# Optimization experiments

Hardware: AMD Instinct MI355X
Metric: run time of the kernel (lower is better)

## Reference

```python
import jax, jax.numpy as jnp
import numpy as np

N_QUBITS = 6
N_QLAYERS = 3
CNOT = jnp.array([[1,0,0,0],[0,1,0,0],[0,0,0,1],[0,0,1,0]], dtype=jnp.complex64).reshape(2,2,2,2)


def _rx(t):
    c = jnp.cos(0.5 * t).astype(jnp.complex64)
    s = jnp.sin(0.5 * t).astype(jnp.complex64)
    return jnp.stack([jnp.stack([c, -1j * s]), jnp.stack([-1j * s, c])])


def _ry(t):
    c = jnp.cos(0.5 * t).astype(jnp.complex64)
    s = jnp.sin(0.5 * t).astype(jnp.complex64)
    return jnp.stack([jnp.stack([c, -s]), jnp.stack([s, c])])


def _rz(t):
    e0 = jnp.exp(-0.5j * t)
    e1 = jnp.exp(0.5j * t)
    z = jnp.zeros((), jnp.complex64)
    return jnp.stack([jnp.stack([e0, z]), jnp.stack([z, e1])])


def _apply1(state, U, wire):
    st = jnp.tensordot(U, state, axes=([1], [wire]))
    return jnp.moveaxis(st, 0, wire)


def _apply_cnot(state, c, t):
    st = jnp.tensordot(CNOT, state, axes=([2, 3], [c, t]))
    return jnp.moveaxis(st, (0, 1), (c, t))


def _circuit(inputs, weights):
    # 6-qubit statevector sim of the PennyLane circuit; inputs: [6], weights: [3,6]
    state = jnp.zeros((2,) * N_QUBITS, jnp.complex64).at[(0,) * N_QUBITS].set(1.0)
    for i in range(N_QUBITS):
        state = _apply1(state, _rx(inputs[i % N_QUBITS]), i)
        state = _apply1(state, _ry(inputs[(i + 1) % N_QUBITS]), i)
        state = _apply1(state, _rz(inputs[(i + 2) % N_QUBITS]), i)
    for _l in range(N_QLAYERS):
        for q in range(N_QUBITS):
            state = _apply1(state, _ry(weights[_l, q]), q)
        for q in range(N_QUBITS):
            state = _apply_cnot(state, q, (q + 1) % N_QUBITS)
    probs = jnp.abs(state) ** 2
    zvec = jnp.array([1.0, -1.0], jnp.float32)
    return jnp.stack([jnp.tensordot(probs, zvec, axes=([i], [0])).sum() for i in range(N_QUBITS)])


def _forward(x, cw1, cb1, cw2, cb2, cw3, cb3, W_ih, W_hh, b_ih, b_hh, q_weights, Wq, bq, Wo, bo):
    h = jnp.transpose(x, (0, 2, 1))  # [B, F, T]
    for W, b in ((cw1, cb1), (cw2, cb2), (cw3, cb3)):
        h = jax.lax.conv_general_dilated(h, W, (1,), [(1, 1)], dimension_numbers=('NCH', 'OIH', 'NCH')) + b[None, :, None]
        h = jax.nn.relu(h)
    tcn_out = jnp.transpose(h, (0, 2, 1))  # [B, T, H]
    B, H = x.shape[0], tcn_out.shape[2]
    qbatch = jax.vmap(lambda inp: _circuit(inp, q_weights))

    def step(carry, x_t):
        hx, cx = carry
        gates = x_t @ W_ih.T + b_ih + hx @ W_hh.T + b_hh
        i_g, f_g, g_g, o_g = jnp.split(gates, 4, axis=1)
        c = jax.nn.sigmoid(f_g) * cx + jax.nn.sigmoid(i_g) * jnp.tanh(g_g)
        hh = jax.nn.sigmoid(o_g) * jnp.tanh(c)
        hh = 3.99 * hh * (1.0 - hh)  # logistic map
        x_new = 1.0 - 1.4 * hh[:, 0] ** 2 + hh[:, 1]  # henon map on dims 0,1
        y_new = 0.3 * hh[:, 0]
        hh = jnp.concatenate([x_new[:, None], y_new[:, None], hh[:, 2:]], axis=1)
        q = qbatch(hh[:, :N_QUBITS])  # [B, 6]
        hh = hh + q @ Wq.T + bq  # QuantumRNNCell(hx, hx)
        return (hh, c), None

    step = jax.checkpoint(step)
    hx = jnp.zeros((B, H), x.dtype)
    cx = jnp.zeros((B, H), x.dtype)
    (hx, cx), _ = jax.lax.scan(step, (hx, cx), jnp.swapaxes(tcn_out, 0, 1))
    return jax.nn.sigmoid(hx @ Wo.T + bo)  # [B, 1]


def setup_inputs() -> dict:
    key = jax.random.key(0)
    ks = jax.random.split(key, 20)
    B, T, F, H = 4096, 256, 32, 32

    def u(k, shape, fan):
        s = 1.0 / np.sqrt(fan)
        return jax.random.uniform(k, shape, jnp.float32, -s, s)

    return {
        'x': jax.random.normal(ks[0], (B, T, F), jnp.float32),
        'cw1': u(ks[1], (H, F, 3), F * 3), 'cb1': u(ks[2], (H,), F * 3),
        'cw2': u(ks[3], (H, H, 3), H * 3), 'cb2': u(ks[4], (H,), H * 3),
        'cw3': u(ks[5], (H, H, 3), H * 3), 'cb3': u(ks[6], (H,), H * 3),
        'W_ih': u(ks[7], (4 * H, H), H), 'W_hh': u(ks[8], (4 * H, H), H),
        'b_ih': u(ks[9], (4 * H,), H), 'b_hh': u(ks[10], (4 * H,), H),
        'q_weights': jax.random.uniform(ks[11], (N_QLAYERS, N_QUBITS), jnp.float32, 0.0, 2.0 * np.pi),
        'Wq': u(ks[12], (H, N_QUBITS), N_QUBITS), 'bq': u(ks[13], (H,), N_QUBITS),
        'Wo': u(ks[14], (1, H), H), 'bo': u(ks[15], (1,), H),
    }


def reference(x, cw1, cb1, cw2, cb2, cw3, cb3, W_ih, W_hh, b_ih, b_hh, q_weights, Wq, bq, Wo, bo):
    return _forward(x, cw1, cb1, cw2, cb2, cw3, cb3, W_ih, W_hh, b_ih, b_hh, q_weights, Wq, bq, Wo, bo)
```

## Files before the change

### kernel.cpp

```cpp
#include <hip/hip_runtime.h>

#define B_TOT 4096
#define T_LEN 256
#define NCH   32

typedef float f2 __attribute__((ext_vector_type(2)));
typedef float f4 __attribute__((ext_vector_type(4)));

__device__ __forceinline__ float rdlane(float v, int l) {
    return __int_as_float(__builtin_amdgcn_readlane(__float_as_int(v), l));
}
__device__ __forceinline__ float xor1f(float x) {
    return __int_as_float(__builtin_amdgcn_mov_dpp(__float_as_int(x), 0xB1, 0xF, 0xF, true));
}
__device__ __forceinline__ float xor2f(float x) {
    return __int_as_float(__builtin_amdgcn_mov_dpp(__float_as_int(x), 0x4E, 0xF, 0xF, true));
}
__device__ __forceinline__ float xor3f(float x) {
    return __int_as_float(__builtin_amdgcn_mov_dpp(__float_as_int(x), 0x1B, 0xF, 0xF, true));
}
__device__ __forceinline__ float xor8f(float x) {
    return __int_as_float(__builtin_amdgcn_mov_dpp(__float_as_int(x), 0x128, 0xF, 0xF, true));
}
__device__ __forceinline__ float xsign(float x, unsigned m) {
    return __int_as_float(__float_as_int(x) ^ (int)m);
}
__device__ __forceinline__ float fast_sig(float x) {
    return __builtin_amdgcn_rcpf(1.0f + __expf(-x));
}
__device__ __forceinline__ float fast_tanh(float x) {
    return fmaf(-2.0f, __builtin_amdgcn_rcpf(__expf(2.0f * x) + 1.0f), 1.0f);
}

__device__ __forceinline__ void fast_sincos(float x, float& s, float& c) {
    float k = rintf(x * 0.3183098861837907f);
    float r = fmaf(-k, 3.14159274101257324f, x);
    r = fmaf(-k, -8.74227765734758577e-8f, r);
    float r2 = r * r;
    float sp = fmaf(-2.50521084e-8f, r2, 2.75573192e-6f);
    sp = fmaf(sp, r2, -1.98412698e-4f);
    sp = fmaf(sp, r2, 8.33333333e-3f);
    sp = fmaf(sp, r2, -1.66666667e-1f);
    float sv = fmaf(sp * r2, r, r);
    float cp = fmaf(2.08767570e-9f, r2, -2.75573192e-7f);
    cp = fmaf(cp, r2, 2.48015873e-5f);
    cp = fmaf(cp, r2, -1.38888889e-3f);
    cp = fmaf(cp, r2, 4.16666667e-2f);
    cp = fmaf(cp, r2, -0.5f);
    float cv = fmaf(cp, r2, 1.0f);
    float sgn = ((int)k & 1) ? -1.0f : 1.0f;
    s = sv * sgn;
    c = cv * sgn;
}

__device__ __forceinline__ void sincos_poly(float x, float& s, float& c) {
    float r2 = x * x;
    float sp = fmaf(-2.50521084e-8f, r2, 2.75573192e-6f);
    sp = fmaf(sp, r2, -1.98412698e-4f);
    sp = fmaf(sp, r2, 8.33333333e-3f);
    sp = fmaf(sp, r2, -1.66666667e-1f);
    s = fmaf(sp * r2, x, x);
    float cp = fmaf(2.08767570e-9f, r2, -2.75573192e-7f);
    cp = fmaf(cp, r2, 2.48015873e-5f);
    cp = fmaf(cp, r2, -1.38888889e-3f);
    cp = fmaf(cp, r2, 4.16666667e-2f);
    cp = fmaf(cp, r2, -0.5f);
    c = fmaf(cp, r2, 1.0f);
}

__global__ __launch_bounds__(256) void tcn_kernel(
    const float* __restrict__ x,
    const float* __restrict__ cw1, const float* __restrict__ cb1,
    const float* __restrict__ cw2, const float* __restrict__ cb2,
    const float* __restrict__ cw3, const float* __restrict__ cb3,
    float* __restrict__ out)
{
    __shared__ float bufA[NCH * 258];
    __shared__ float bufB[NCH * 258];
    __shared__ float sW[NCH * 97];
    __shared__ float sB[NCH];

    const int b   = blockIdx.x;
    const int tid = threadIdx.x;
    const float* xb = x + (size_t)b * T_LEN * NCH;

    #pragma unroll
    for (int c = 0; c < 32; ++c) {
        int idx = c * 256 + tid;
        int t = idx >> 5, f = idx & 31;
        bufA[f * 258 + t] = xb[idx];
    }
    __syncthreads();

    float* bin  = bufA;
    float* bout = bufB;
    const int o  = tid & 31;
    const int t0 = (tid >> 5) * 32;

    for (int layer = 0; layer < 3; ++layer) {
        const float* Wg = (layer == 0) ? cw1 : ((layer == 1) ? cw2 : cw3);
        const float* Bg = (layer == 0) ? cb1 : ((layer == 1) ? cb2 : cb3);
        for (int idx = tid; idx < 32 * 96; idx += 256) {
            int oo = idx / 96, rem = idx - oo * 96;
            sW[oo * 97 + rem] = Wg[idx];
        }
        if (tid < 32) sB[tid] = Bg[tid];
        __syncthreads();

        f2 acc2[16];
        const float bias = sB[o];
        #pragma unroll
        for (int j = 0; j < 16; ++j) acc2[j] = f2{bias, bias};

        for (int i = 0; i < 32; ++i) {
            const float w0 = sW[o * 97 + i * 3 + 0];
            const float w1 = sW[o * 97 + i * 3 + 1];
            const float w2 = sW[o * 97 + i * 3 + 2];
            const float* row = bin + i * 258;
            const f2* rp = (const f2*)(row + t0);
            float vmE = (t0 == 0)   ? 0.0f : row[t0 - 1];
            float vpE = (t0 == 224) ? 0.0f : row[t0 + 32];
            f2 Lprev = f2{0.0f, 0.0f};
            f2 Lcur  = rp[0];
            #pragma unroll
            for (int j = 0; j < 16; ++j) {
                f2 Lnext = (j < 15) ? rp[j + 1] : f2{vpE, 0.0f};
                f2 vm = (j == 0) ? f2{vmE, Lcur.x}
                                 : __builtin_shufflevector(Lprev, Lcur, 1, 2);
                f2 vp = __builtin_shufflevector(Lcur, Lnext, 1, 2);
                acc2[j] = __builtin_elementwise_fma(f2{w0, w0}, vm,   acc2[j]);
                acc2[j] = __builtin_elementwise_fma(f2{w1, w1}, Lcur, acc2[j]);
                acc2[j] = __builtin_elementwise_fma(f2{w2, w2}, vp,   acc2[j]);
                Lprev = Lcur; Lcur = Lnext;
            }
        }
        f2* wout = (f2*)(bout + o * 258 + t0);
        #pragma unroll
        for (int j = 0; j < 16; ++j) {
            f2 r;
            r.x = fmaxf(acc2[j].x, 0.0f);
            r.y = fmaxf(acc2[j].y, 0.0f);
            wout[j] = r;
        }
        __syncthreads();
        float* tmp = bin; bin = bout; bout = tmp;
    }

    float* og = out + (size_t)b * T_LEN * NCH;
    #pragma unroll
    for (int c = 0; c < 32; ++c) {
        int idx = c * 256 + tid;
        int t = idx >> 5, f = idx & 31;
        og[idx] = bin[f * 258 + t];
    }
}

__global__ __launch_bounds__(64, 2) void scan_kernel(
    const float* __restrict__ tcn,
    const float* __restrict__ W_ih, const float* __restrict__ W_hh,
    const float* __restrict__ b_ih, const float* __restrict__ b_hh,
    const float* __restrict__ qw,
    const float* __restrict__ Wq, const float* __restrict__ bq,
    const float* __restrict__ Wo, const float* __restrict__ bo,
    float* __restrict__ out)
{
    __shared__ __align__(16) float xcA[64], xcB[64];
    __shared__ __align__(16) float colA[24], colB[24];

    const int lane = threadIdx.x;
    const int b2   = blockIdx.x * 2;
    const float* xrowA = tcn + (size_t)b2 * T_LEN * NCH;
    const float* xrowB = xrowA + T_LEN * NCH;

    f2 wih[32], whh[32];
    #pragma unroll
    for (int k = 0; k < 32; ++k) {
        wih[k] = f2{ W_ih[lane * 32 + k], W_ih[(lane + 64) * 32 + k] };
        whh[k] = f2{ W_hh[lane * 32 + k], W_hh[(lane + 64) * 32 + k] };
    }
    const f2 bias01 = f2{ b_ih[lane] + b_hh[lane],
                          b_ih[lane + 64] + b_hh[lane + 64] };

    float ssu[18], ccu[18];
    {
        float s0, c0;
        int j = (lane < 18) ? lane : 0;
        fast_sincos(0.5f * qw[j], s0, c0);
        #pragma unroll
        for (int i = 0; i < 18; ++i) { ssu[i] = rdlane(s0, i); ccu[i] = rdlane(c0, i); }
    }
    float vs1 = ssu[0], vc1 = ccu[0];
    #pragma unroll
    for (int i = 1; i < 6; ++i) {
        vs1 = (lane == i) ? ssu[i] : vs1;
        vc1 = (lane == i) ? ccu[i] : vc1;
    }
    const int MU2[6] = {31, 48, 56, 60, 62, 63};
    const int MU3[6] = {53, 47, 23, 43, 21, 42};
    float ssl2[6], ssl3[6], cc2[6], cc3[6];
    #pragma unroll
    for (int q = 0; q < 6; ++q) {
        ssl2[q] = (__popc(lane & MU2[q]) & 1) ? ssu[6 + q]  : -ssu[6 + q];
        ssl3[q] = (__popc(lane & MU3[q]) & 1) ? ssu[12 + q] : -ssu[12 + q];
        cc2[q] = ccu[6 + q];
        cc3[q] = ccu[12 + q];
    }
    unsigned nm[6];
    #pragma unroll
    for (int q = 0; q < 6; ++q) nm[q] = (lane & (32 >> q)) ? 0u : 0x80000000u;
    int cidx[6];
    #pragma unroll
    for (int i = 0; i < 6; ++i) cidx[i] = i * 2 + ((lane & (32 >> i)) ? 1 : 0);
    const int r1 = (lane + 1) % 6, r2 = (lane + 2) % 6;

    float wqr[6] = {0, 0, 0, 0, 0, 0};
    float bqr = 0.0f, wor = 0.0f;
    if (lane < 32) {
        #pragma unroll
        for (int k = 0; k < 6; ++k) wqr[k] = Wq[lane * 6 + k];
        bqr = bq[lane];
        wor = Wo[lane];
    }

    float hhA = 0.0f, cellA = 0.0f, hhB = 0.0f, cellB = 0.0f;
    float xpA = (lane < 32) ? xrowA[lane] : 0.0f;
    float xpB = (lane < 32) ? xrowB[lane] : 0.0f;

    const f4* xqA = (const f4*)xcA;
    const f4* xqB = (const f4*)xcB;
    const f2* clA = (const f2*)colA;
    const f2* clB = (const f2*)colB;

    for (int t = 0; t < T_LEN; ++t) {
        if (lane < 32) {
            ((f2*)xcA)[lane] = f2{xpA, hhA};
            ((f2*)xcB)[lane] = f2{xpB, hhB};
        }
        float xnA = (lane < 32 && t < T_LEN - 1) ? xrowA[(t + 1) * 32 + lane] : 0.0f;
        float xnB = (lane < 32 && t < T_LEN - 1) ? xrowB[(t + 1) * 32 + lane] : 0.0f;

        f2 aA = bias01, bA_ = f2{0.0f, 0.0f};
        f2 aB = bias01, bB_ = f2{0.0f, 0.0f};
        #pragma unroll
        for (int j = 0; j < 16; ++j) {
            f4 vA = xqA[j], vB = xqB[j];
            aA  = __builtin_elementwise_fma(wih[2*j],   __builtin_shufflevector(vA, vA, 0, 0), aA);
            aB  = __builtin_elementwise_fma(wih[2*j],   __builtin_shufflevector(vB, vB, 0, 0), aB);
            aA  = __builtin_elementwise_fma(whh[2*j],   __builtin_shufflevector(vA, vA, 1, 1), aA);
            aB  = __builtin_elementwise_fma(whh[2*j],   __builtin_shufflevector(vB, vB, 1, 1), aB);
            bA_ = __builtin_elementwise_fma(wih[2*j+1], __builtin_shufflevector(vA, vA, 2, 2), bA_);
            bB_ = __builtin_elementwise_fma(wih[2*j+1], __builtin_shufflevector(vB, vB, 2, 2), bB_);
            bA_ = __builtin_elementwise_fma(whh[2*j+1], __builtin_shufflevector(vA, vA, 3, 3), bA_);
            bB_ = __builtin_elementwise_fma(whh[2*j+1], __builtin_shufflevector(vB, vB, 3, 3), bB_);
        }
        aA += bA_; aB += bB_;
        float acc0A = aA.x, acc1A = aA.y;
        float acc0B = aB.x, acc1B = aB.y;

        float fgA = __shfl_xor(acc0A, 32, 64), ogA = __shfl_xor(acc1A, 32, 64);
        float fgB = __shfl_xor(acc0B, 32, 64), ogB = __shfl_xor(acc1B, 32, 64);
        float cA = fast_sig(fgA) * cellA + fast_sig(acc0A) * fast_tanh(acc1A);
        float cB = fast_sig(fgB) * cellB + fast_sig(acc0B) * fast_tanh(acc1B);
        float hA = fast_sig(ogA) * fast_tanh(cA);
        float hB = fast_sig(ogB) * fast_tanh(cB);
        hA = 3.99f * hA * (1.0f - hA);
        hB = 3.99f * hB * (1.0f - hB);
        float h0A = rdlane(hA, 0), h1A = rdlane(hA, 1);
        float h0B = rdlane(hB, 0), h1B = rdlane(hB, 1);
        float henA0 = fmaf(-1.4f * h0A, h0A, 1.0f) + h1A;
        float henB0 = fmaf(-1.4f * h0B, h0B, 1.0f) + h1B;
        hA = (lane == 0) ? henA0 : hA;
        hB = (lane == 0) ? henB0 : hB;
        hA = (lane == 1) ? 0.3f * h0A : hA;
        hB = (lane == 1) ? 0.3f * h0B : hB;
        cellA = cA; cellB = cB;

        float sOA, cOA, sOB, cOB;
        sincos_poly(0.5f * hA, sOA, cOA);
        sincos_poly(0.5f * hB, sOB, cOB);
        float s1A = __shfl(sOA, r1, 64), c1A = __shfl(cOA, r1, 64);
        float s1B = __shfl(sOB, r1, 64), c1B = __shfl(cOB, r1, 64);
        float s2A = __shfl(sOA, r2, 64), c2A = __shfl(cOA, r2, 64);
        float s2B = __shfl(sOB, r2, 64), c2B = __shfl(cOB, r2, 64);
        {
            float A_ = c1A * cOA, Bv = s1A * sOA;
            float C_ = s1A * cOA, D_ = c1A * sOA;
            float ur = fmaf(Bv, s2A,  A_ * c2A);
            float ui = fmaf(Bv, c2A, -(A_ * s2A));
            float pr = fmaf(D_, s2A,  C_ * c2A);
            float pi = fmaf(C_, s2A, -(D_ * c2A));
            float nur = fmaf(vc1, ur, -(vs1 * pr));
            float nui = fmaf(vc1, ui, -(vs1 * pi));
            float npr = fmaf(vs1, ur,  vc1 * pr);
            float npi = fmaf(vs1, ui,  vc1 * pi);
            if (lane < 6) *(f4*)&colA[lane * 4] = f4{nur, nui, npr, npi};
        }
        {
            float A_ = c1B * cOB, Bv = s1B * sOB;
            float C_ = s1B * cOB, D_ = c1B * sOB;
            float ur = fmaf(Bv, s2B,  A_ * c2B);
            float ui = fmaf(Bv, c2B, -(A_ * s2B));
            float pr = fmaf(D_, s2B,  C_ * c2B);
            float pi = fmaf(C_, s2B, -(D_ * c2B));
            float nur = fmaf(vc1, ur, -(vs1 * pr));
            float nui = fmaf(vc1, ui, -(vs1 * pi));
            float npr = fmaf(vs1, ur,  vc1 * pr);
            float npi = fmaf(vs1, ui,  vc1 * pi);
            if (lane < 6) *(f4*)&colB[lane * 4] = f4{nur, nui, npr, npi};
        }

        f2 gA0 = clA[cidx[0]], gB0 = clB[cidx[0]];
        float reA = gA0.x, imA = gA0.y;
        float reB = gB0.x, imB = gB0.y;
        #pragma unroll
        for (int i = 1; i < 6; ++i) {
            f2 gA = clA[cidx[i]], gB = clB[cidx[i]];
            float nrA = fmaf(reA, gA.x, -(imA * gA.y));
            float niA = fmaf(reA, gA.y,   imA * gA.x);
            float nrB = fmaf(reB, gB.x, -(imB * gB.y));
            float niB = fmaf(reB, gB.y,   imB * gB.x);
            reA = nrA; imA = niA; reB = nrB; imB = niB;
        }

        {
            float pA, qA, pB, qB;
            pA = __shfl_xor(reA, 48, 64); qA = __shfl_xor(imA, 48, 64);
            pB = __shfl_xor(reB, 48, 64); qB = __shfl_xor(imB, 48, 64);
            reA = fmaf(ssl2[0], pA, cc2[0] * reA); imA = fmaf(ssl2[0], qA, cc2[0] * imA);
            reB = fmaf(ssl2[0], pB, cc2[0] * reB); imB = fmaf(ssl2[0], qB, cc2[0] * imB);
            pA = __shfl_xor(reA, 24, 64); qA = __shfl_xor(imA, 24, 64);
            pB = __shfl_xor(reB, 24, 64); qB = __shfl_xor(imB, 24, 64);
            reA = fmaf(ssl2[1], pA, cc2[1] * reA); imA = fmaf(ssl2[1], qA, cc2[1] * imA);
            reB = fmaf(ssl2[1], pB, cc2[1] * reB); imB = fmaf(ssl2[1], qB, cc2[1] * imB);
            pA = __shfl_xor(reA, 12, 64); qA = __shfl_xor(imA, 12, 64);
            pB = __shfl_xor(reB, 12, 64); qB = __shfl_xor(imB, 12, 64);
            reA = fmaf(ssl2[2], pA, cc2[2] * reA); imA = fmaf(ssl2[2], qA, cc2[2] * imA);
            reB = fmaf(ssl2[2], pB, cc2[2] * reB); imB = fmaf(ssl2[2], qB, cc2[2] * imB);
            pA = __shfl_xor(reA, 6, 64);  qA = __shfl_xor(imA, 6, 64);
            pB = __shfl_xor(reB, 6, 64);  qB = __shfl_xor(imB, 6, 64);
            reA = fmaf(ssl2[3], pA, cc2[3] * reA); imA = fmaf(ssl2[3], qA, cc2[3] * imA);
            reB = fmaf(ssl2[3], pB, cc2[3] * reB); imB = fmaf(ssl2[3], qB, cc2[3] * imB);
            pA = xor3f(reA); qA = xor3f(imA);
            pB = xor3f(reB); qB = xor3f(imB);
            reA = fmaf(ssl2[4], pA, cc2[4] * reA); imA = fmaf(ssl2[4], qA, cc2[4] * imA);
            reB = fmaf(ssl2[4], pB, cc2[4] * reB); imB = fmaf(ssl2[4], qB, cc2[4] * imB);
            pA = __shfl_xor(reA, 49, 64); qA = __shfl_xor(imA, 49, 64);
            pB = __shfl_xor(reB, 49, 64); qB = __shfl_xor(imB, 49, 64);
            reA = fmaf(ssl2[5], pA, cc2[5] * reA); imA = fmaf(ssl2[5], qA, cc2[5] * imA);
            reB = fmaf(ssl2[5], pB, cc2[5] * reB); imB = fmaf(ssl2[5], qB, cc2[5] * imB);
        }
        {
            float pA, qA, pB, qB;
            pA = __shfl_xor(reA, 40, 64); qA = __shfl_xor(imA, 40, 64);
            pB = __shfl_xor(reB, 40, 64); qB = __shfl_xor(imB, 40, 64);
            reA = fmaf(ssl3[0], pA, cc3[0] * reA); imA = fmaf(ssl3[0], qA, cc3[0] * imA);
            reB = fmaf(ssl3[0], pB, cc3[0] * reB); imB = fmaf(ssl3[0], qB, cc3[0] * imB);
            pA = __shfl_xor(reA, 20, 64); qA = __shfl_xor(imA, 20, 64);
            pB = __shfl_xor(reB, 20, 64); qB = __shfl_xor(imB, 20, 64);
            reA = fmaf(ssl3[1], pA, cc3[1] * reA); imA = fmaf(ssl3[1], qA, cc3[1] * imA);
            reB = fmaf(ssl3[1], pB, cc3[1] * reB); imB = fmaf(ssl3[1], qB, cc3[1] * imB);
            pA = __shfl_xor(reA, 10, 64); qA = __shfl_xor(imA, 10, 64);
            pB = __shfl_xor(reB, 10, 64); qB = __shfl_xor(imB, 10, 64);
            reA = fmaf(ssl3[2], pA, cc3[2] * reA); imA = fmaf(ssl3[2], qA, cc3[2] * imA);
            reB = fmaf(ssl3[2], pB, cc3[2] * reB); imB = fmaf(ssl3[2], qB, cc3[2] * imB);
            pA = __shfl_xor(reA, 5, 64);  qA = __shfl_xor(imA, 5, 64);
            pB = __shfl_xor(reB, 5, 64);  qB = __shfl_xor(imB, 5, 64);
            reA = fmaf(ssl3[3], pA, cc3[3] * reA); imA = fmaf(ssl3[3], qA, cc3[3] * imA);
            reB = fmaf(ssl3[3], pB, cc3[3] * reB); imB = fmaf(ssl3[3], qB, cc3[3] * imB);
            pA = __shfl_xor(reA, 50, 64); qA = __shfl_xor(imA, 50, 64);
            pB = __shfl_xor(reB, 50, 64); qB = __shfl_xor(imB, 50, 64);
            reA = fmaf(ssl3[4], pA, cc3[4] * reA); imA = fmaf(ssl3[4], qA, cc3[4] * imA);
            reB = fmaf(ssl3[4], pB, cc3[4] * reB); imB = fmaf(ssl3[4], qB, cc3[4] * imB);
            pA = __shfl_xor(reA, 25, 64); qA = __shfl_xor(imA, 25, 64);
            pB = __shfl_xor(reB, 25, 64); qB = __shfl_xor(imB, 25, 64);
            reA = fmaf(ssl3[5], pA, cc3[5] * reA); imA = fmaf(ssl3[5], qA, cc3[5] * imA);
            reB = fmaf(ssl3[5], pB, cc3[5] * reB); imB = fmaf(ssl3[5], qB, cc3[5] * imB);
        }

        float pA = fmaf(reA, reA, imA * imA);
        float pB = fmaf(reB, reB, imB * imB);
        { float tA = xor1f(pA), tB = xor1f(pB);
          pA = tA - xsign(pA, nm[5]); pB = tB - xsign(pB, nm[5]); }
        { float tA = xor2f(pA), tB = xor2f(pB);
          pA = tA - xsign(pA, nm[4]); pB = tB - xsign(pB, nm[4]); }
        { float tA = __shfl_xor(pA, 4, 64), tB = __shfl_xor(pB, 4, 64);
          pA = tA - xsign(pA, nm[3]); pB = tB - xsign(pB, nm[3]); }
        { float tA = xor8f(pA), tB = xor8f(pB);
          pA = tA - xsign(pA, nm[2]); pB = tB - xsign(pB, nm[2]); }
        { float tA = __shfl_xor(pA, 16, 64), tB = __shfl_xor(pB, 16, 64);
          pA = tA - xsign(pA, nm[1]); pB = tB - xsign(pB, nm[1]); }
        { float tA = __shfl_xor(pA, 32, 64), tB = __shfl_xor(pB, 32, 64);
          pA = tA - xsign(pA, nm[0]); pB = tB - xsign(pB, nm[0]); }

        float updA = bqr, updB = bqr;
        updA = fmaf(rdlane(pA, 44), wqr[0], updA); updB = fmaf(rdlane(pB, 44), wqr[0], updB);
        updA = fmaf(rdlane(pA, 26), wqr[1], updA); updB = fmaf(rdlane(pB, 26), wqr[1], updB);
        updA = fmaf(rdlane(pA, 13), wqr[2], updA); updB = fmaf(rdlane(pB, 13), wqr[2], updB);
        updA = fmaf(rdlane(pA, 38), wqr[3], updA); updB = fmaf(rdlane(pB, 38), wqr[3], updB);
        updA = fmaf(rdlane(pA, 51), wqr[4], updA); updB = fmaf(rdlane(pB, 51), wqr[4], updB);
        updA = fmaf(rdlane(pA, 25), wqr[5], updA); updB = fmaf(rdlane(pB, 25), wqr[5], updB);
        hhA = hA + updA;
        hhB = hB + updB;
        xpA = xnA; xpB = xnB;
    }

    float cA = (lane < 32) ? hhA * wor : 0.0f;
    float cB = (lane < 32) ? hhB * wor : 0.0f;
    #pragma unroll
    for (int off = 32; off >= 1; off >>= 1) {
        cA += __shfl_xor(cA, off, 64);
        cB += __shfl_xor(cB, off, 64);
    }
    if (lane == 0) {
        float bo0 = bo[0];
        out[b2]     = fast_sig(cA + bo0);
        out[b2 + 1] = fast_sig(cB + bo0);
    }
}

extern "C" void kernel_launch(void* const* d_in, const int* in_sizes, int n_in,
                              void* d_out, int out_size, void* d_ws, size_t ws_size,
                              hipStream_t stream)
{
    const float* x    = (const float*)d_in[0];
    const float* cw1  = (const float*)d_in[1];
    const float* cb1  = (const float*)d_in[2];
    const float* cw2  = (const float*)d_in[3];
    const float* cb2  = (const float*)d_in[4];
    const float* cw3  = (const float*)d_in[5];
    const float* cb3  = (const float*)d_in[6];
    const float* W_ih = (const float*)d_in[7];
    const float* W_hh = (const float*)d_in[8];
    const float* b_ih = (const float*)d_in[9];
    const float* b_hh = (const float*)d_in[10];
    const float* qw   = (const float*)d_in[11];
    const float* Wq   = (const float*)d_in[12];
    const float* bq   = (const float*)d_in[13];
    const float* Wo   = (const float*)d_in[14];
    const float* bo   = (const float*)d_in[15];

    float* tcn = (float*)d_ws;

    hipLaunchKernelGGL(tcn_kernel, dim3(B_TOT), dim3(256), 0, stream,
                       x, cw1, cb1, cw2, cb2, cw3, cb3, tcn);
    hipLaunchKernelGGL(scan_kernel, dim3(B_TOT / 2), dim3(64), 0, stream,
                       tcn, W_ih, W_hh, b_ih, b_hh, qw, Wq, bq, Wo, bo,
                       (float*)d_out);
}
```

Measured before the change: 996.4 us.

## Read LSTM inputs directly from global and broadcast qubit columns via readlane

The per-step LSTM inputs are now loaded directly from global memory (uniform addresses, likely scalar loads) instead of being staged through shared memory with a prefetch register. The hidden state for both sequences is packed into a single shared buffer. The per-qubit product-state column values, previously written to shared memory by lanes 0-5 and gathered back, are now broadcast with readlane and selected per lane. Together these remove LDS round trips and their wait latency from the serial scan loop, at the cost of more readlane and scalar-load traffic on the critical path.

```diff
diff --git a/kernel.cpp b/kernel.cpp
--- a/kernel.cpp
+++ b/kernel.cpp
@@ -164,8 +164,7 @@
     const float* __restrict__ Wo, const float* __restrict__ bo,
     float* __restrict__ out)
 {
-    __shared__ __align__(16) float xcA[64], xcB[64];
-    __shared__ __align__(16) float colA[24], colB[24];
+    __shared__ __align__(16) float hb[64];
 
     const int lane = threadIdx.x;
     const int b2   = blockIdx.x * 2;
@@ -208,9 +207,6 @@
     unsigned nm[6];
     #pragma unroll
     for (int q = 0; q < 6; ++q) nm[q] = (lane & (32 >> q)) ? 0u : 0x80000000u;
-    int cidx[6];
-    #pragma unroll
-    for (int i = 0; i < 6; ++i) cidx[i] = i * 2 + ((lane & (32 >> i)) ? 1 : 0);
     const int r1 = (lane + 1) % 6, r2 = (lane + 2) % 6;
 
     float wqr[6] = {0, 0, 0, 0, 0, 0};
@@ -223,35 +219,28 @@
     }
 
     float hhA = 0.0f, cellA = 0.0f, hhB = 0.0f, cellB = 0.0f;
-    float xpA = (lane < 32) ? xrowA[lane] : 0.0f;
-    float xpB = (lane < 32) ? xrowB[lane] : 0.0f;
-
-    const f4* xqA = (const f4*)xcA;
-    const f4* xqB = (const f4*)xcB;
-    const f2* clA = (const f2*)colA;
-    const f2* clB = (const f2*)colB;
+    const f4* hq = (const f4*)hb;
 
     for (int t = 0; t < T_LEN; ++t) {
-        if (lane < 32) {
-            ((f2*)xcA)[lane] = f2{xpA, hhA};
-            ((f2*)xcB)[lane] = f2{xpB, hhB};
-        }
-        float xnA = (lane < 32 && t < T_LEN - 1) ? xrowA[(t + 1) * 32 + lane] : 0.0f;
-        float xnB = (lane < 32 && t < T_LEN - 1) ? xrowB[(t + 1) * 32 + lane] : 0.0f;
+        if (lane < 32) ((f2*)hb)[lane] = f2{hhA, hhB};
+        const float* xA = xrowA + t * 32;
+        const float* xB = xrowB + t * 32;
 
         f2 aA = bias01, bA_ = f2{0.0f, 0.0f};
         f2 aB = bias01, bB_ = f2{0.0f, 0.0f};
         #pragma unroll
         for (int j = 0; j < 16; ++j) {
-            f4 vA = xqA[j], vB = xqB[j];
-            aA  = __builtin_elementwise_fma(wih[2*j],   __builtin_shufflevector(vA, vA, 0, 0), aA);
-            aB  = __builtin_elementwise_fma(wih[2*j],   __builtin_shufflevector(vB, vB, 0, 0), aB);
-            aA  = __builtin_elementwise_fma(whh[2*j],   __builtin_shufflevector(vA, vA, 1, 1), aA);
-            aB  = __builtin_elementwise_fma(whh[2*j],   __builtin_shufflevector(vB, vB, 1, 1), aB);
-            bA_ = __builtin_elementwise_fma(wih[2*j+1], __builtin_shufflevector(vA, vA, 2, 2), bA_);
-            bB_ = __builtin_elementwise_fma(wih[2*j+1], __builtin_shufflevector(vB, vB, 2, 2), bB_);
-            bA_ = __builtin_elementwise_fma(whh[2*j+1], __builtin_shufflevector(vA, vA, 3, 3), bA_);
-            bB_ = __builtin_elementwise_fma(whh[2*j+1], __builtin_shufflevector(vB, vB, 3, 3), bB_);
+            f4 hv = hq[j];
+            float x0A = xA[2 * j], x1A = xA[2 * j + 1];
+            float x0B = xB[2 * j], x1B = xB[2 * j + 1];
+            aA  = __builtin_elementwise_fma(wih[2*j],   f2{x0A, x0A},   aA);
+            aA  = __builtin_elementwise_fma(whh[2*j],   f2{hv.x, hv.x}, aA);
+            bA_ = __builtin_elementwise_fma(wih[2*j+1], f2{x1A, x1A},   bA_);
+            bA_ = __builtin_elementwise_fma(whh[2*j+1], f2{hv.z, hv.z}, bA_);
+            aB  = __builtin_elementwise_fma(wih[2*j],   f2{x0B, x0B},   aB);
+            aB  = __builtin_elementwise_fma(whh[2*j],   f2{hv.y, hv.y}, aB);
+            bB_ = __builtin_elementwise_fma(wih[2*j+1], f2{x1B, x1B},   bB_);
+            bB_ = __builtin_elementwise_fma(whh[2*j+1], f2{hv.w, hv.w}, bB_);
         }
         aA += bA_; aB += bB_;
         float acc0A = aA.x, acc1A = aA.y;
@@ -282,6 +271,7 @@
         float s1B = __shfl(sOB, r1, 64), c1B = __shfl(cOB, r1, 64);
         float s2A = __shfl(sOA, r2, 64), c2A = __shfl(cOA, r2, 64);
         float s2B = __shfl(sOB, r2, 64), c2B = __shfl(cOB, r2, 64);
+        float nurA, nuiA, nprA, npiA, nurB, nuiB, nprB, npiB;
         {
             float A_ = c1A * cOA, Bv = s1A * sOA;
             float C_ = s1A * cOA, D_ = c1A * sOA;
@@ -289,11 +279,10 @@
             float ui = fmaf(Bv, c2A, -(A_ * s2A));
             float pr = fmaf(D_, s2A,  C_ * c2A);
             float pi = fmaf(C_, s2A, -(D_ * c2A));
-            float nur = fmaf(vc1, ur, -(vs1 * pr));
-            float nui = fmaf(vc1, ui, -(vs1 * pi));
-            float npr = fmaf(vs1, ur,  vc1 * pr);
-            float npi = fmaf(vs1, ui,  vc1 * pi);
-            if (lane < 6) *(f4*)&colA[lane * 4] = f4{nur, nui, npr, npi};
+            nurA = fmaf(vc1, ur, -(vs1 * pr));
+            nuiA = fmaf(vc1, ui, -(vs1 * pi));
+            nprA = fmaf(vs1, ur,  vc1 * pr);
+            npiA = fmaf(vs1, ui,  vc1 * pi);
         }
         {
             float A_ = c1B * cOB, Bv = s1B * sOB;
@@ -302,23 +291,35 @@
             float ui = fmaf(Bv, c2B, -(A_ * s2B));
             float pr = fmaf(D_, s2B,  C_ * c2B);
             float pi = fmaf(C_, s2B, -(D_ * c2B));
-            float nur = fmaf(vc1, ur, -(vs1 * pr));
-            float nui = fmaf(vc1, ui, -(vs1 * pi));
-            float npr = fmaf(vs1, ur,  vc1 * pr);
-            float npi = fmaf(vs1, ui,  vc1 * pi);
-            if (lane < 6) *(f4*)&colB[lane * 4] = f4{nur, nui, npr, npi};
-        }
-
-        f2 gA0 = clA[cidx[0]], gB0 = clB[cidx[0]];
-        float reA = gA0.x, imA = gA0.y;
-        float reB = gB0.x, imB = gB0.y;
+            nurB = fmaf(vc1, ur, -(vs1 * pr));
+            nuiB = fmaf(vc1, ui, -(vs1 * pi));
+            nprB = fmaf(vs1, ur,  vc1 * pr);
+            npiB = fmaf(vs1, ui,  vc1 * pi);
+        }
+
+        float reA, imA, reB, imB;
+        {
+            bool hi0 = (lane & 32) != 0;
+            float uA = rdlane(nurA, 0), vA = rdlane(nuiA, 0);
+            float pA_ = rdlane(nprA, 0), qA_ = rdlane(npiA, 0);
+            float uB = rdlane(nurB, 0), vB = rdlane(nuiB, 0);
+            float pB_ = rdlane(nprB, 0), qB_ = rdlane(npiB, 0);
+            reA = hi0 ? pA_ : uA;  imA = hi0 ? qA_ : vA;
+            reB = hi0 ? pB_ : uB;  imB = hi0 ? qB_ : vB;
+        }
         #pragma unroll
         for (int i = 1; i < 6; ++i) {
-            f2 gA = clA[cidx[i]], gB = clB[cidx[i]];
-            float nrA = fmaf(reA, gA.x, -(imA * gA.y));
-            float niA = fmaf(reA, gA.y,   imA * gA.x);
-            float nrB = fmaf(reB, gB.x, -(imB * gB.y));
-            float niB = fmaf(reB, gB.y,   imB * gB.x);
+            const bool hi = (lane & (32 >> i)) != 0;
+            float uA = rdlane(nurA, i), vA = rdlane(nuiA, i);
+            float pA_ = rdlane(nprA, i), qA_ = rdlane(npiA, i);
+            float uB = rdlane(nurB, i), vB = rdlane(nuiB, i);
+            float pB_ = rdlane(nprB, i), qB_ = rdlane(npiB, i);
+            float grA = hi ? pA_ : uA, giA = hi ? qA_ : vA;
+            float grB = hi ? pB_ : uB, giB = hi ? qB_ : vB;
+            float nrA = fmaf(reA, grA, -(imA * giA));
+            float niA = fmaf(reA, giA,   imA * grA);
+            float nrB = fmaf(reB, grB, -(imB * giB));
+            float niB = fmaf(reB, giB,   imB * grB);
             reA = nrA; imA = niA; reB = nrB; imB = niB;
         }
 
@@ -401,7 +402,6 @@
         updA = fmaf(rdlane(pA, 25), wqr[5], updA); updB = fmaf(rdlane(pB, 25), wqr[5], updB);
         hhA = hA + updA;
         hhB = hB + updB;
-        xpA = xnA; xpB = xnB;
     }
 
     float cA = (lane < 32) ? hhA * wor : 0.0f;
```

New measurement: 1.088 ms. 1.09x slower.
